# Kernel tuning notes

Hardware: AMD Instinct MI355X
Metric: run time of the kernel (lower is better)

The kernel has to match this reference:

```python
import jax, jax.numpy as jnp
import numpy as np

D_MODEL = 512
N_HEADS = 8
D_K = D_MODEL // N_HEADS
WINDOW = 32  # attention restricted to |i-j| <= WINDOW//2
SCALE = float(np.sqrt(D_K))


def setup_inputs() -> dict:
    key = jax.random.key(0)
    ks = jax.random.split(key, 11)
    B, S, D = 2, 4096, D_MODEL
    inv = 1.0 / np.sqrt(D)
    inp = {
        "query": jax.random.normal(ks[0], (B, S, D), jnp.float32),
        "key": jax.random.normal(ks[1], (B, S, D), jnp.float32),
        "value": jax.random.normal(ks[2], (B, S, D), jnp.float32),
        # torch nn.Linear params: weight (out,in), bias (out,)
        "wq": jax.random.uniform(ks[3], (D, D), jnp.float32, -inv, inv),
        "bq": jax.random.uniform(ks[4], (D,), jnp.float32, -inv, inv),
        "wk": jax.random.uniform(ks[5], (D, D), jnp.float32, -inv, inv),
        "bk": jax.random.uniform(ks[6], (D,), jnp.float32, -inv, inv),
        "wv": jax.random.uniform(ks[7], (D, D), jnp.float32, -inv, inv),
        "bv": jax.random.uniform(ks[8], (D,), jnp.float32, -inv, inv),
        "wo": jax.random.uniform(ks[9], (D, D), jnp.float32, -inv, inv),
        "bo": jax.random.uniform(ks[10], (D,), jnp.float32, -inv, inv),
    }
    return inp


def _linear(x, w, b):
    # torch: y = x @ w.T + b
    return jnp.einsum('bsd,od->bso', x, w) + b


def reference(query, key, value, wq, bq, wk, bk, wv, bv, wo, bo):
    B, S, D = query.shape
    # project and split heads -> [B, H, S, d_k]
    def split(x):
        return x.reshape(B, S, N_HEADS, D_K).transpose(0, 2, 1, 3)
    Q = split(_linear(query, wq, bq))
    K = split(_linear(key, wk, bk))
    V = split(_linear(value, wv, bv))
    # full scores then banded mask (faithful to original dense-masked impl)
    scores = jnp.einsum('bhqd,bhkd->bhqk', Q, K) / SCALE
    i = jnp.arange(S)[:, None]
    j = jnp.arange(S)[None, :]
    band = jnp.abs(i - j) <= (WINDOW // 2)  # [S, S]
    scores = jnp.where(band[None, None, :, :], scores, -1e9)
    attn = jax.nn.softmax(scores, axis=-1)
    ctx = jnp.einsum('bhqk,bhkd->bhqd', attn, V)
    ctx = ctx.transpose(0, 2, 1, 3).reshape(B, S, D)
    return _linear(ctx, wo, bo)
```

## Files before the change

### kernel.cpp

```cpp
#include <hip/hip_runtime.h>
#include <hip/hip_bf16.h>

using u16 = unsigned short;
using u32 = unsigned int;

typedef float f32x4 __attribute__((ext_vector_type(4)));
typedef __bf16 bf16x8 __attribute__((ext_vector_type(8)));

constexpr int B_ = 2;
constexpr int S_ = 4096;
constexpr int D_ = 512;
constexpr int H_ = 8;
constexpr int DK_ = 64;
constexpr int M_ = B_ * S_;
constexpr int K_ = 512;

__device__ __forceinline__ float bf2f(u16 u) {
  return __uint_as_float(((u32)u) << 16);
}
__device__ __forceinline__ u16 f2bf(float x) {
  u32 u = __float_as_uint(x);
  u = (u + 0x7fffu + ((u >> 16) & 1u)) >> 16;
  return (u16)u;
}
__device__ __forceinline__ u32 pack2(float a, float b) {
  return (u32)f2bf(a) | ((u32)f2bf(b) << 16);
}

__device__ __forceinline__ void gload16(const u16* g, u16* l) {
  __builtin_amdgcn_global_load_lds((const __attribute__((address_space(1))) void*)g,
                                   (__attribute__((address_space(3))) void*)l,
                                   16, 0, 0);
}

constexpr int NG_W = 4 * (262144 / 8);

__global__ __launch_bounds__(256) void convert_w(
    const float* __restrict__ wq, const float* __restrict__ wk,
    const float* __restrict__ wv, const float* __restrict__ wo,
    u16* __restrict__ wqb, u16* __restrict__ wkb, u16* __restrict__ wvb,
    u16* __restrict__ wob)
{
  const int g8 = blockIdx.x * 256 + threadIdx.x;
  if (g8 >= NG_W) return;
  const int t = g8 >> 15;
  const int r = g8 & 32767;
  const float* s = (t == 0) ? wq : (t == 1) ? wk : (t == 2) ? wv : wo;
  u16* d = (t == 0) ? wqb : (t == 1) ? wkb : (t == 2) ? wvb : wob;
  const size_t off = (size_t)r * 8;
  const float4 x = *(const float4*)(s + off);
  const float4 y = *(const float4*)(s + off + 4);
  uint4 o;
  o.x = pack2(x.x, x.y); o.y = pack2(x.z, x.w);
  o.z = pack2(y.x, y.y); o.w = pack2(y.z, y.w);
  *(uint4*)(d + off) = o;
}

template<int MODE>
__device__ __forceinline__ void gemm_body_f32A(const float* __restrict__ A,
                                               const u16* __restrict__ Wt,
                                               const float* __restrict__ bias,
                                               void* __restrict__ Cout,
                                               u16* __restrict__ As,
                                               u16* __restrict__ Bs)
{
  const int tid  = threadIdx.x;
  const int lane = tid & 63;
  const int w    = tid >> 6;
  const int wm   = w >> 1;
  const int wn   = w & 1;
  const int m0   = blockIdx.x * 128;
  const int n0   = blockIdx.y * 128;
  const int qr   = lane & 15;
  const int g    = lane >> 4;

  const int sr8 = tid >> 3;
  const int c8  = tid & 7;
  const float* afp = A + (size_t)(m0 + sr8) * K_ + c8 * 8;
  char* awr = (char*)As + sr8 * 128 + ((c8 ^ (sr8 & 7)) * 16);

  auto a_load = [&](int t, int p, float4& x, float4& y) {
    const float* s = afp + t * 64 + (size_t)p * 32 * K_;
    x = *(const float4*)s;
    y = *(const float4*)(s + 4);
  };
  auto a_write = [&](int p, const float4& x, const float4& y) {
    uint4 o;
    o.x = pack2(x.x, x.y); o.y = pack2(x.z, x.w);
    o.z = pack2(y.x, y.y); o.w = pack2(y.z, y.w);
    *(uint4*)(awr + p * 32 * 128) = o;
  };

  const int swz8 = ((lane & 7) ^ (lane >> 3)) * 8;
  const u16* b0 = Wt + (size_t)(n0 + w * 32 + (lane >> 3)) * K_ + swz8;
  auto stage_B = [&](int t) {
#pragma unroll
    for (int p = 0; p < 4; ++p)
      gload16(b0 + t * 64 + (size_t)p * 8 * K_, &Bs[(w * 32 + p * 8) * 64]);
  };

  f32x4 acc[4][4] = {};

  {
    float4 x0, y0, x1, y1, x2, y2, x3, y3;
    a_load(0, 0, x0, y0); a_load(0, 1, x1, y1);
    a_load(0, 2, x2, y2); a_load(0, 3, x3, y3);
    a_write(0, x0, y0); a_write(1, x1, y1);
    a_write(2, x2, y2); a_write(3, x3, y3);
    stage_B(0);
  }

  const int ax = (qr & 7) << 4;
  const char* ab = (const char*)As + (wm * 64 + qr) * 128;
  const char* bb = (const char*)Bs + (wn * 64 + qr) * 128;

  constexpr int NT = K_ / 64;
#pragma unroll 1
  for (int t = 0; t < NT; ++t) {
    __syncthreads();

    float4 xa, ya, xb, yb;
    if (t + 1 < NT) {
      a_load(t + 1, 0, xa, ya);
      a_load(t + 1, 1, xb, yb);
    }

#pragma unroll
    for (int kk = 0; kk < 2; ++kk) {
      bf16x8 af[4], bfr[4];
#pragma unroll
      for (int i = 0; i < 4; ++i)
        af[i]  = *(const bf16x8*)(ab + i * 2048 + ((g * 16 + kk * 64) ^ ax));
#pragma unroll
      for (int j = 0; j < 4; ++j)
        bfr[j] = *(const bf16x8*)(bb + j * 2048 + ((g * 16 + kk * 64) ^ ax));
#pragma unroll
      for (int i = 0; i < 4; ++i)
#pragma unroll
        for (int j = 0; j < 4; ++j)
          acc[i][j] = __builtin_amdgcn_mfma_f32_16x16x32_bf16(af[i], bfr[j], acc[i][j], 0, 0, 0);
    }

    if (t + 1 < NT) {
      __syncthreads();
      a_write(0, xa, ya); a_write(1, xb, yb);
      float4 xc, yc, xd, yd;
      a_load(t + 1, 2, xc, yc); a_load(t + 1, 3, xd, yd);
      a_write(2, xc, yc); a_write(3, xd, yd);
      stage_B(t + 1);
    }
  }

#pragma unroll
  for (int j = 0; j < 4; ++j) {
    const int col = n0 + wn * 64 + j * 16 + qr;
    const float bv = bias[col];
#pragma unroll
    for (int i = 0; i < 4; ++i) {
      const int rbase = m0 + wm * 64 + i * 16 + g * 4;
      if constexpr (MODE == 2) {
        const int bb2 = rbase >> 12;
        const int ss = rbase & (S_ - 1);
        const int hh = col >> 6;
        const int dd = col & (DK_ - 1);
        uint2 pk;
        pk.x = pack2(acc[i][j][0] + bv, acc[i][j][1] + bv);
        pk.y = pack2(acc[i][j][2] + bv, acc[i][j][3] + bv);
        *(uint2*)&((u16*)Cout)[((size_t)((bb2 * H_ + hh) * DK_ + dd)) * S_ + ss] = pk;
      } else {
#pragma unroll
        for (int r = 0; r < 4; ++r) {
          const int row = rbase + r;
          const int bb2 = row >> 12;
          const int ss = row & (S_ - 1);
          const int hh = col >> 6;
          const int dd = col & (DK_ - 1);
          ((u16*)Cout)[((size_t)(bb2 * H_ + hh) * S_ + ss) * DK_ + dd] =
              f2bf(acc[i][j][r] + bv);
        }
      }
    }
  }
}

__global__ __launch_bounds__(256, 4) void gemm_qkv(
    const float* __restrict__ q, const float* __restrict__ k, const float* __restrict__ v,
    const u16* __restrict__ wqb, const u16* __restrict__ wkb, const u16* __restrict__ wvb,
    const float* __restrict__ bq, const float* __restrict__ bk, const float* __restrict__ bv,
    u16* __restrict__ Qo, u16* __restrict__ Ko, u16* __restrict__ Vo)
{
  __shared__ u16 As[128 * 64];
  __shared__ u16 Bs[128 * 64];
  if (blockIdx.z == 0)      gemm_body_f32A<1>(q, wqb, bq, Qo, As, Bs);
  else if (blockIdx.z == 1) gemm_body_f32A<1>(k, wkb, bk, Ko, As, Bs);
  else                      gemm_body_f32A<2>(v, wvb, bv, Vo, As, Bs);
}

__global__ __launch_bounds__(256, 4) void gemm_out(
    const u16* __restrict__ A, const u16* __restrict__ Wt,
    const float* __restrict__ bias, float* __restrict__ C)
{
  __shared__ u16 As[128 * 64];
  __shared__ u16 Bs[128 * 64];

  const int tid  = threadIdx.x;
  const int lane = tid & 63;
  const int w    = tid >> 6;
  const int wm   = w >> 1;
  const int wn   = w & 1;
  const int m0   = blockIdx.x * 128;
  const int n0   = blockIdx.y * 128;
  const int qr   = lane & 15;
  const int g    = lane >> 4;

  const int swz8 = ((lane & 7) ^ (lane >> 3)) * 8;
  const u16* a0 = A  + (size_t)(m0 + w * 32 + (lane >> 3)) * K_ + swz8;
  const u16* b0 = Wt + (size_t)(n0 + w * 32 + (lane >> 3)) * K_ + swz8;

  auto stage = [&](int t) {
#pragma unroll
    for (int p = 0; p < 4; ++p)
      gload16(a0 + t * 64 + (size_t)p * 8 * K_, &As[(w * 32 + p * 8) * 64]);
#pragma unroll
    for (int p = 0; p < 4; ++p)
      gload16(b0 + t * 64 + (size_t)p * 8 * K_, &Bs[(w * 32 + p * 8) * 64]);
  };

  f32x4 acc[4][4] = {};
  stage(0);

  const int ax = (qr & 7) << 4;
  const char* ab = (const char*)As + (wm * 64 + qr) * 128;
  const char* bb = (const char*)Bs + (wn * 64 + qr) * 128;

  constexpr int NT = K_ / 64;
#pragma unroll 1
  for (int t = 0; t < NT; ++t) {
    __syncthreads();
#pragma unroll
    for (int kk = 0; kk < 2; ++kk) {
      bf16x8 af[4], bfr[4];
#pragma unroll
      for (int i = 0; i < 4; ++i)
        af[i]  = *(const bf16x8*)(ab + i * 2048 + ((g * 16 + kk * 64) ^ ax));
#pragma unroll
      for (int j = 0; j < 4; ++j)
        bfr[j] = *(const bf16x8*)(bb + j * 2048 + ((g * 16 + kk * 64) ^ ax));
#pragma unroll
      for (int i = 0; i < 4; ++i)
#pragma unroll
        for (int j = 0; j < 4; ++j)
          acc[i][j] = __builtin_amdgcn_mfma_f32_16x16x32_bf16(af[i], bfr[j], acc[i][j], 0, 0, 0);
    }
    if (t + 1 < NT) {
      __syncthreads();
      stage(t + 1);
    }
  }

#pragma unroll
  for (int j = 0; j < 4; ++j) {
    const int col = n0 + wn * 64 + j * 16 + qr;
    const float bv = bias[col];
#pragma unroll
    for (int i = 0; i < 4; ++i) {
      const int rbase = m0 + wm * 64 + i * 16 + g * 4;
#pragma unroll
      for (int r = 0; r < 4; ++r)
        C[(size_t)(rbase + r) * D_ + col] = acc[i][j][r] + bv;
    }
  }
}

__global__ __launch_bounds__(256) void attn_band_mfma(
    const u16* __restrict__ Q, const u16* __restrict__ K,
    const u16* __restrict__ Vt, u16* __restrict__ Ctx)
{
  constexpr int LDP = 72;
  __shared__ u16 P_lds[4][16 * LDP];

  const int lane = threadIdx.x & 63;
  const int w    = threadIdx.x >> 6;
  const int wid  = blockIdx.x * 4 + w;
  const int q0   = (wid & 255) << 4;
  const int bh   = wid >> 8;
  const size_t kbase = (size_t)bh * S_ * DK_;

  u16* pl = &P_lds[w][0];
  const int qr = lane & 15;
  const int g  = lane >> 4;

  *(uint2*)&pl[qr * LDP + 48 + 4 * g] = make_uint2(0u, 0u);

  bf16x8 qf[2];
  {
    const u16* qp = Q + kbase + (size_t)(q0 + qr) * DK_ + 8 * g;
    qf[0] = *(const bf16x8*)qp;
    qf[1] = *(const bf16x8*)(qp + 32);
  }

  f32x4 sc[3];
#pragma unroll
  for (int t = 0; t < 3; ++t) {
    int j = q0 - 16 + 16 * t + qr;
    j = min(max(j, 0), S_ - 1);
    const u16* kp = K + kbase + (size_t)j * DK_ + 8 * g;
    const bf16x8 kf0 = *(const bf16x8*)kp;
    const bf16x8 kf1 = *(const bf16x8*)(kp + 32);
    f32x4 a = {};
    a = __builtin_amdgcn_mfma_f32_16x16x32_bf16(kf0, qf[0], a, 0, 0, 0);
    a = __builtin_amdgcn_mfma_f32_16x16x32_bf16(kf1, qf[1], a, 0, 0, 0);
    sc[t] = a;
  }

  float s[3][4];
  float mx = -INFINITY;
#pragma unroll
  for (int t = 0; t < 3; ++t)
#pragma unroll
    for (int r = 0; r < 4; ++r) {
      const int joff = 16 * t + 4 * g + r;
      const int j = q0 - 16 + joff;
      const bool ok = (joff >= qr) && (joff <= qr + 32) && (j >= 0) && (j < S_);
      const float v = ok ? sc[t][r] * 0.125f : -INFINITY;
      s[t][r] = v;
      mx = fmaxf(mx, v);
    }
  mx = fmaxf(mx, __shfl_xor(mx, 16));
  mx = fmaxf(mx, __shfl_xor(mx, 32));

  float p[3][4];
  float den = 0.f;
#pragma unroll
  for (int t = 0; t < 3; ++t)
#pragma unroll
    for (int r = 0; r < 4; ++r) {
      p[t][r] = __expf(s[t][r] - mx);
      den += p[t][r];
    }
  den += __shfl_xor(den, 16);
  den += __shfl_xor(den, 32);
  const float inv = 1.0f / den;

#pragma unroll
  for (int t = 0; t < 3; ++t) {
    uint2 pk;
    pk.x = pack2(p[t][0] * inv, p[t][1] * inv);
    pk.y = pack2(p[t][2] * inv, p[t][3] * inv);
    *(uint2*)&pl[qr * LDP + 16 * t + 4 * g] = pk;
  }

  f32x4 cacc[4] = {};
#pragma unroll
  for (int jc = 0; jc < 2; ++jc) {
    const bf16x8 pa = *(const bf16x8*)&pl[qr * LDP + 8 * g + 32 * jc];
#pragma unroll
    for (int nt = 0; nt < 4; ++nt) {
      int jj = q0 - 16 + 8 * g + 32 * jc;
      jj = min(max(jj, 0), S_ - 8);
      const u16* vp = Vt + ((size_t)bh * DK_ + 16 * nt + qr) * S_ + jj;
      const bf16x8 vf = *(const bf16x8*)vp;
      cacc[nt] = __builtin_amdgcn_mfma_f32_16x16x32_bf16(pa, vf, cacc[nt], 0, 0, 0);
    }
  }

  const int bb = bh >> 3;
  const int hh = bh & (H_ - 1);
#pragma unroll
  for (int nt = 0; nt < 4; ++nt)
#pragma unroll
    for (int r = 0; r < 4; ++r) {
      const int qq = 4 * g + r;
      const int dd = 16 * nt + qr;
      Ctx[((size_t)(bb * S_ + q0 + qq)) * D_ + hh * DK_ + dd] = f2bf(cacc[nt][r]);
    }
}

extern "C" void kernel_launch(void* const* d_in, const int* in_sizes, int n_in,
                              void* d_out, int out_size, void* d_ws, size_t ws_size,
                              hipStream_t stream)
{
  const float* query = (const float*)d_in[0];
  const float* key   = (const float*)d_in[1];
  const float* value = (const float*)d_in[2];
  const float* wq    = (const float*)d_in[3];
  const float* bq    = (const float*)d_in[4];
  const float* wk    = (const float*)d_in[5];
  const float* bk    = (const float*)d_in[6];
  const float* wv    = (const float*)d_in[7];
  const float* bv    = (const float*)d_in[8];
  const float* wo    = (const float*)d_in[9];
  const float* bo    = (const float*)d_in[10];

  const size_t seg = (size_t)M_ * D_;
  u16* Qw  = (u16*)d_ws;
  u16* Kw  = Qw + seg;
  u16* Vw  = Kw + seg;
  u16* Cw  = Vw + seg;
  u16* wqb = Cw + seg;
  u16* wkb = wqb + (size_t)D_ * D_;
  u16* wvb = wkb + (size_t)D_ * D_;
  u16* wob = wvb + (size_t)D_ * D_;

  dim3 blk(256);
  convert_w<<<dim3((NG_W + 255) / 256), blk, 0, stream>>>(
      wq, wk, wv, wo, wqb, wkb, wvb, wob);
  gemm_qkv<<<dim3(M_ / 128, D_ / 128, 3), blk, 0, stream>>>(
      query, key, value, wqb, wkb, wvb, bq, bk, bv, Qw, Kw, Vw);
  attn_band_mfma<<<dim3((B_ * H_ * S_) / 64), blk, 0, stream>>>(Qw, Kw, Vw, Cw);
  gemm_out<<<dim3(M_ / 128, D_ / 128), blk, 0, stream>>>(Cw, wob, bo, (float*)d_out);
}
```

Baseline: 68.54 us.

## Stage fp32 activations via direct LDS loads, row-major Q/K, smaller output tiles

The QKV GEMM now copies fp32 activation tiles straight into LDS with global_load_lds and converts them to bf16 with v_cvt_pk_bf16_f32 at fragment-read time, instead of staging through registers and packing in software. This removes register round-trips and the VALU packing work, but doubles the A-tile LDS footprint and lowers the occupancy hint. Q and K are now written row-major [B,S,D] rather than head-split, so stores coalesce, and the attention kernel indexes them accordingly. The output GEMM uses 64-row tiles to double the number of blocks and fill more CUs.

Result: faster. 56.88 us (-17.0%).

```diff
diff --git a/kernel.cpp b/kernel.cpp
--- a/kernel.cpp
+++ b/kernel.cpp
@@ -26,8 +26,13 @@
 __device__ __forceinline__ u32 pack2(float a, float b) {
   return (u32)f2bf(a) | ((u32)f2bf(b) << 16);
 }
-
-__device__ __forceinline__ void gload16(const u16* g, u16* l) {
+__device__ __forceinline__ u32 cvtpk(float a, float b) {
+  u32 r;
+  asm("v_cvt_pk_bf16_f32 %0, %1, %2" : "=v"(r) : "v"(a), "v"(b));
+  return r;
+}
+
+__device__ __forceinline__ void gload16(const void* g, void* l) {
   __builtin_amdgcn_global_load_lds((const __attribute__((address_space(1))) void*)g,
                                    (__attribute__((address_space(3))) void*)l,
                                    16, 0, 0);
@@ -57,12 +62,12 @@
 }
 
 template<int MODE>
-__device__ __forceinline__ void gemm_body_f32A(const float* __restrict__ A,
-                                               const u16* __restrict__ Wt,
-                                               const float* __restrict__ bias,
-                                               void* __restrict__ Cout,
-                                               u16* __restrict__ As,
-                                               u16* __restrict__ Bs)
+__device__ __forceinline__ void gemm_qkv_body(const float* __restrict__ A,
+                                              const u16* __restrict__ Wt,
+                                              const float* __restrict__ bias,
+                                              void* __restrict__ Cout,
+                                              float* __restrict__ Asf,
+                                              u16* __restrict__ Bs)
 {
   const int tid  = threadIdx.x;
   const int lane = tid & 63;
@@ -74,21 +79,18 @@
   const int qr   = lane & 15;
   const int g    = lane >> 4;
 
-  const int sr8 = tid >> 3;
-  const int c8  = tid & 7;
-  const float* afp = A + (size_t)(m0 + sr8) * K_ + c8 * 8;
-  char* awr = (char*)As + sr8 * 128 + ((c8 ^ (sr8 & 7)) * 16);
-
-  auto a_load = [&](int t, int p, float4& x, float4& y) {
-    const float* s = afp + t * 64 + (size_t)p * 32 * K_;
-    x = *(const float4*)s;
-    y = *(const float4*)(s + 4);
-  };
-  auto a_write = [&](int p, const float4& x, const float4& y) {
-    uint4 o;
-    o.x = pack2(x.x, x.y); o.y = pack2(x.z, x.w);
-    o.z = pack2(y.x, y.y); o.w = pack2(y.z, y.w);
-    *(uint4*)(awr + p * 32 * 128) = o;
+  const int r4 = lane >> 4;
+  const int c4 = (lane & 15) * 4;
+  const int colx0 = c4 ^ (r4 << 3);
+  const int colx1 = colx0 ^ 32;
+  const float* arow = A + (size_t)(m0 + w * 32 + r4) * K_;
+
+  auto stage_A = [&](int t) {
+    const float* base = arow + t * 64;
+#pragma unroll
+    for (int p = 0; p < 8; ++p)
+      gload16(base + (size_t)(p * 4) * K_ + ((p & 1) ? colx1 : colx0),
+              Asf + (w * 32 + p * 4) * 64);
   };
 
   const int swz8 = ((lane & 7) ^ (lane >> 3)) * 8;
@@ -101,39 +103,39 @@
 
   f32x4 acc[4][4] = {};
 
-  {
-    float4 x0, y0, x1, y1, x2, y2, x3, y3;
-    a_load(0, 0, x0, y0); a_load(0, 1, x1, y1);
-    a_load(0, 2, x2, y2); a_load(0, 3, x3, y3);
-    a_write(0, x0, y0); a_write(1, x1, y1);
-    a_write(2, x2, y2); a_write(3, x3, y3);
-    stage_B(0);
-  }
-
-  const int ax = (qr & 7) << 4;
-  const char* ab = (const char*)As + (wm * 64 + qr) * 128;
+  stage_A(0);
+  stage_B(0);
+
+  const int ax5 = (qr & 7) << 5;
+  const int ax4 = (qr & 7) << 4;
+  const char* ab = (const char*)Asf + (wm * 64 + qr) * 256;
   const char* bb = (const char*)Bs + (wn * 64 + qr) * 128;
+
+  union U8 { u32 u[4]; bf16x8 v; };
 
   constexpr int NT = K_ / 64;
 #pragma unroll 1
   for (int t = 0; t < NT; ++t) {
     __syncthreads();
 
-    float4 xa, ya, xb, yb;
-    if (t + 1 < NT) {
-      a_load(t + 1, 0, xa, ya);
-      a_load(t + 1, 1, xb, yb);
-    }
-
 #pragma unroll
     for (int kk = 0; kk < 2; ++kk) {
       bf16x8 af[4], bfr[4];
 #pragma unroll
-      for (int i = 0; i < 4; ++i)
-        af[i]  = *(const bf16x8*)(ab + i * 2048 + ((g * 16 + kk * 64) ^ ax));
+      for (int i = 0; i < 4; ++i) {
+        const char* p = ab + i * 4096 + ((g * 32 + kk * 128) ^ ax5);
+        const f32x4 lo = *(const f32x4*)p;
+        const f32x4 hi = *(const f32x4*)(p + 16);
+        U8 u;
+        u.u[0] = cvtpk(lo[0], lo[1]);
+        u.u[1] = cvtpk(lo[2], lo[3]);
+        u.u[2] = cvtpk(hi[0], hi[1]);
+        u.u[3] = cvtpk(hi[2], hi[3]);
+        af[i] = u.v;
+      }
 #pragma unroll
       for (int j = 0; j < 4; ++j)
-        bfr[j] = *(const bf16x8*)(bb + j * 2048 + ((g * 16 + kk * 64) ^ ax));
+        bfr[j] = *(const bf16x8*)(bb + j * 2048 + ((g * 16 + kk * 64) ^ ax4));
 #pragma unroll
       for (int i = 0; i < 4; ++i)
 #pragma unroll
@@ -143,10 +145,7 @@
 
     if (t + 1 < NT) {
       __syncthreads();
-      a_write(0, xa, ya); a_write(1, xb, yb);
-      float4 xc, yc, xd, yd;
-      a_load(t + 1, 2, xc, yc); a_load(t + 1, 3, xd, yd);
-      a_write(2, xc, yc); a_write(3, xd, yd);
+      stage_A(t + 1);
       stage_B(t + 1);
     }
   }
@@ -169,38 +168,31 @@
         *(uint2*)&((u16*)Cout)[((size_t)((bb2 * H_ + hh) * DK_ + dd)) * S_ + ss] = pk;
       } else {
 #pragma unroll
-        for (int r = 0; r < 4; ++r) {
-          const int row = rbase + r;
-          const int bb2 = row >> 12;
-          const int ss = row & (S_ - 1);
-          const int hh = col >> 6;
-          const int dd = col & (DK_ - 1);
-          ((u16*)Cout)[((size_t)(bb2 * H_ + hh) * S_ + ss) * DK_ + dd] =
-              f2bf(acc[i][j][r] + bv);
-        }
+        for (int r = 0; r < 4; ++r)
+          ((u16*)Cout)[(size_t)(rbase + r) * D_ + col] = f2bf(acc[i][j][r] + bv);
       }
     }
   }
 }
 
-__global__ __launch_bounds__(256, 4) void gemm_qkv(
+__global__ __launch_bounds__(256, 3) void gemm_qkv(
     const float* __restrict__ q, const float* __restrict__ k, const float* __restrict__ v,
     const u16* __restrict__ wqb, const u16* __restrict__ wkb, const u16* __restrict__ wvb,
     const float* __restrict__ bq, const float* __restrict__ bk, const float* __restrict__ bv,
     u16* __restrict__ Qo, u16* __restrict__ Ko, u16* __restrict__ Vo)
 {
-  __shared__ u16 As[128 * 64];
-  __shared__ u16 Bs[128 * 64];
-  if (blockIdx.z == 0)      gemm_body_f32A<1>(q, wqb, bq, Qo, As, Bs);
-  else if (blockIdx.z == 1) gemm_body_f32A<1>(k, wkb, bk, Ko, As, Bs);
-  else                      gemm_body_f32A<2>(v, wvb, bv, Vo, As, Bs);
-}
-
-__global__ __launch_bounds__(256, 4) void gemm_out(
+  __shared__ float Asf[128 * 64];
+  __shared__ u16   Bs[128 * 64];
+  if (blockIdx.z == 0)      gemm_qkv_body<0>(q, wqb, bq, Qo, Asf, Bs);
+  else if (blockIdx.z == 1) gemm_qkv_body<0>(k, wkb, bk, Ko, Asf, Bs);
+  else                      gemm_qkv_body<2>(v, wvb, bv, Vo, Asf, Bs);
+}
+
+__global__ __launch_bounds__(256, 2) void gemm_out(
     const u16* __restrict__ A, const u16* __restrict__ Wt,
     const float* __restrict__ bias, float* __restrict__ C)
 {
-  __shared__ u16 As[128 * 64];
+  __shared__ u16 As[64 * 64];
   __shared__ u16 Bs[128 * 64];
 
   const int tid  = threadIdx.x;
@@ -208,29 +200,29 @@
   const int w    = tid >> 6;
   const int wm   = w >> 1;
   const int wn   = w & 1;
-  const int m0   = blockIdx.x * 128;
+  const int m0   = blockIdx.x * 64;
   const int n0   = blockIdx.y * 128;
   const int qr   = lane & 15;
   const int g    = lane >> 4;
 
   const int swz8 = ((lane & 7) ^ (lane >> 3)) * 8;
-  const u16* a0 = A  + (size_t)(m0 + w * 32 + (lane >> 3)) * K_ + swz8;
+  const u16* a0 = A  + (size_t)(m0 + w * 16 + (lane >> 3)) * K_ + swz8;
   const u16* b0 = Wt + (size_t)(n0 + w * 32 + (lane >> 3)) * K_ + swz8;
 
   auto stage = [&](int t) {
 #pragma unroll
-    for (int p = 0; p < 4; ++p)
-      gload16(a0 + t * 64 + (size_t)p * 8 * K_, &As[(w * 32 + p * 8) * 64]);
+    for (int p = 0; p < 2; ++p)
+      gload16(a0 + t * 64 + (size_t)p * 8 * K_, &As[(w * 16 + p * 8) * 64]);
 #pragma unroll
     for (int p = 0; p < 4; ++p)
       gload16(b0 + t * 64 + (size_t)p * 8 * K_, &Bs[(w * 32 + p * 8) * 64]);
   };
 
-  f32x4 acc[4][4] = {};
+  f32x4 acc[2][4] = {};
   stage(0);
 
   const int ax = (qr & 7) << 4;
-  const char* ab = (const char*)As + (wm * 64 + qr) * 128;
+  const char* ab = (const char*)As + (wm * 32 + qr) * 128;
   const char* bb = (const char*)Bs + (wn * 64 + qr) * 128;
 
   constexpr int NT = K_ / 64;
@@ -239,15 +231,15 @@
     __syncthreads();
 #pragma unroll
     for (int kk = 0; kk < 2; ++kk) {
-      bf16x8 af[4], bfr[4];
-#pragma unroll
-      for (int i = 0; i < 4; ++i)
+      bf16x8 af[2], bfr[4];
+#pragma unroll
+      for (int i = 0; i < 2; ++i)
         af[i]  = *(const bf16x8*)(ab + i * 2048 + ((g * 16 + kk * 64) ^ ax));
 #pragma unroll
       for (int j = 0; j < 4; ++j)
         bfr[j] = *(const bf16x8*)(bb + j * 2048 + ((g * 16 + kk * 64) ^ ax));
 #pragma unroll
-      for (int i = 0; i < 4; ++i)
+      for (int i = 0; i < 2; ++i)
 #pragma unroll
         for (int j = 0; j < 4; ++j)
           acc[i][j] = __builtin_amdgcn_mfma_f32_16x16x32_bf16(af[i], bfr[j], acc[i][j], 0, 0, 0);
@@ -263,8 +255,8 @@
     const int col = n0 + wn * 64 + j * 16 + qr;
     const float bv = bias[col];
 #pragma unroll
-    for (int i = 0; i < 4; ++i) {
-      const int rbase = m0 + wm * 64 + i * 16 + g * 4;
+    for (int i = 0; i < 2; ++i) {
+      const int rbase = m0 + wm * 32 + i * 16 + g * 4;
 #pragma unroll
       for (int r = 0; r < 4; ++r)
         C[(size_t)(rbase + r) * D_ + col] = acc[i][j][r] + bv;
@@ -284,7 +276,8 @@
   const int wid  = blockIdx.x * 4 + w;
   const int q0   = (wid & 255) << 4;
   const int bh   = wid >> 8;
-  const size_t kbase = (size_t)bh * S_ * DK_;
+  const int bb   = bh >> 3;
+  const int hh   = bh & (H_ - 1);
 
   u16* pl = &P_lds[w][0];
   const int qr = lane & 15;
@@ -294,7 +287,7 @@
 
   bf16x8 qf[2];
   {
-    const u16* qp = Q + kbase + (size_t)(q0 + qr) * DK_ + 8 * g;
+    const u16* qp = Q + ((size_t)(bb * S_ + q0 + qr)) * D_ + hh * DK_ + 8 * g;
     qf[0] = *(const bf16x8*)qp;
     qf[1] = *(const bf16x8*)(qp + 32);
   }
@@ -304,7 +297,7 @@
   for (int t = 0; t < 3; ++t) {
     int j = q0 - 16 + 16 * t + qr;
     j = min(max(j, 0), S_ - 1);
-    const u16* kp = K + kbase + (size_t)j * DK_ + 8 * g;
+    const u16* kp = K + ((size_t)(bb * S_ + j)) * D_ + hh * DK_ + 8 * g;
     const bf16x8 kf0 = *(const bf16x8*)kp;
     const bf16x8 kf1 = *(const bf16x8*)(kp + 32);
     f32x4 a = {};
@@ -364,8 +357,6 @@
     }
   }
 
-  const int bb = bh >> 3;
-  const int hh = bh & (H_ - 1);
 #pragma unroll
   for (int nt = 0; nt < 4; ++nt)
 #pragma unroll
@@ -408,5 +399,5 @@
   gemm_qkv<<<dim3(M_ / 128, D_ / 128, 3), blk, 0, stream>>>(
       query, key, value, wqb, wkb, wvb, bq, bk, bv, Qw, Kw, Vw);
   attn_band_mfma<<<dim3((B_ * H_ * S_) / 64), blk, 0, stream>>>(Qw, Kw, Vw, Cw);
-  gemm_out<<<dim3(M_ / 128, D_ / 128), blk, 0, stream>>>(Cw, wob, bo, (float*)d_out);
-}
+  gemm_out<<<dim3(M_ / 64, D_ / 128), blk, 0, stream>>>(Cw, wob, bo, (float*)d_out);
+}
```
